# Optimization experiments

Hardware: AMD Instinct MI355X
Metric: run time of the kernel (lower is better)

## Reference

```python
import jax, jax.numpy as jnp
import numpy as np

P = 16      # spatial_size
STEP = 8    # spatial_size // 2 (overlapping)
T = 16      # temporal_size


def setup_inputs() -> dict:
    key = jax.random.key(0)
    k1, k2 = jax.random.split(key)
    inp = jax.random.normal(k1, (8, 4, T, 256, 256), dtype=jnp.float32)
    # reset_parameters: uniform(-1/sqrt(spatial_size), 1/sqrt(spatial_size)) = +/-0.25
    weight = jax.random.uniform(k2, (T, STEP, STEP), dtype=jnp.float32,
                                minval=-0.25, maxval=0.25)
    return {"input": inp, "weight": weight,
            "pad_h": 264, "pad_w": 264, "n_patch_h": 32, "n_patch_w": 32}


def reference(input, weight, pad_h, pad_w, n_patch_h, n_patch_w):
    B, S, Tt, H, W = input.shape
    # zero-pad frames to (pad_h, pad_w) = step*(n_patch+1)
    padded = jnp.pad(input, ((0, 0), (0, 0), (0, 0), (0, pad_h - H), (0, pad_w - W)))
    # tile the (T, step, step) mask over the padded frame
    w_tiled = jnp.tile(weight, (1, n_patch_h + 1, n_patch_w + 1))  # (T, pad_h, pad_w)
    # masked multiply + temporal sum  -> (B, S, pad_h, pad_w)
    out = jnp.einsum('bsthw,thw->bshw', padded, w_tiled)
    # overlapping unfold: windows of size P with stride STEP
    wins_h = (pad_h - P) // STEP + 1
    wins_w = (pad_w - P) // STEP + 1
    rows = (jnp.arange(wins_h) * STEP)[:, None] + jnp.arange(P)  # (wins_h, P)
    cols = (jnp.arange(wins_w) * STEP)[:, None] + jnp.arange(P)  # (wins_w, P)
    # gather patches: (B, S, wins_h, wins_w, P, P)
    patches = out[:, :, rows[:, None, :, None], cols[None, :, None, :]]
    # torch permute(0,1,2,3,5,4): transpose each patch
    patches = jnp.swapaxes(patches, 4, 5)
    # view (B, S*wins_h*wins_w, P*P)
    return patches.reshape(B, -1, P * P)
```

## Files before the change

### kernel.cpp

```cpp
#include <hip/hip_runtime.h>


namespace {

constexpr int TT   = 16;
constexpr int LDSW = 268;

__global__ __launch_bounds__(256, 4) void meas_kernel(
    const float* __restrict__ in, const float* __restrict__ wt,
    float* __restrict__ out)
{
    __shared__ float tile[8 * LDSW];
    __shared__ float wlds[TT * 64];

    const int tid = threadIdx.x;
    for (int idx = tid; idx < TT * 64; idx += 256) wlds[idx] = wt[idx];

    if (tid < 16) {
        const int r  = tid >> 1;
        const int c4 = 64 + (tid & 1);
        *reinterpret_cast<float4*>(&tile[r * LDSW + c4 * 4]) =
            make_float4(0.f, 0.f, 0.f, 0.f);
    }

    const int bid = (blockIdx.x & 7) * 128 + (blockIdx.x >> 3);
    const int g = bid & 31;
    const int s = (bid >> 5) & 3;
    const int b = bid >> 7;

    const float* __restrict__ inp = in + (size_t)(b * 4 + s) * TT * 65536;
    float* __restrict__ outb = out + ((size_t)b * 4096 + (size_t)s * 1024) * 256;

    __syncthreads();

#pragma unroll 1
    for (int m = 0; m < 2; ++m) {
        const int slot = m * 256 + tid;
        const int r = slot >> 6;
        const int c = slot & 63;
        const int h = g * 8 + r;
        const int w = c * 4;
        const float* gp = inp + h * 256 + w;

        float4 v[TT];
#pragma unroll
        for (int t = 0; t < TT; ++t)
            v[t] = *reinterpret_cast<const float4*>(gp + t * 65536);

        __builtin_amdgcn_sched_barrier(0);

        const float* wrow = &wlds[(h & 7) * 8 + (w & 7)];
        float4 acc = make_float4(0.f, 0.f, 0.f, 0.f);
#pragma unroll
        for (int t = 0; t < TT; ++t) {
            const float4 wv = *reinterpret_cast<const float4*>(wrow + t * 64);
            acc.x += v[t].x * wv.x;
            acc.y += v[t].y * wv.y;
            acc.z += v[t].z * wv.z;
            acc.w += v[t].w * wv.w;
        }
        *reinterpret_cast<float4*>(&tile[r * LDSW + w]) = acc;
    }

    __syncthreads();

#pragma unroll
    for (int m2 = 0; m2 < 4; ++m2) {
        const int f  = m2 * 256 + tid;
        const int j  = f >> 5;
        const int e  = f & 31;
        const int q2 = e >> 1;
        const int pp = (e & 1) * 4;
        const float* src = &tile[pp * LDSW + j * 8 + q2];
        const float4 a4 = make_float4(src[0], src[LDSW], src[2 * LDSW], src[3 * LDSW]);

        {
            const int n = 32 * g + j;
            *reinterpret_cast<float4*>(outb + (size_t)n * 256 + q2 * 16 + pp) = a4;
        }
        if (g > 0) {
            const int n = 32 * (g - 1) + j;
            *reinterpret_cast<float4*>(outb + (size_t)n * 256 + q2 * 16 + 8 + pp) = a4;
        }
        if (g == 31) {
            const int n = 992 + j;
            *reinterpret_cast<float4*>(outb + (size_t)n * 256 + q2 * 16 + 8 + pp) =
                make_float4(0.f, 0.f, 0.f, 0.f);
        }
    }
}

}

extern "C" void kernel_launch(void* const* d_in, const int* in_sizes, int n_in,
                              void* d_out, int out_size, void* d_ws, size_t ws_size,
                              hipStream_t stream) {
    const float* in = (const float*)d_in[0];
    const float* wt = (const float*)d_in[1];
    float* out      = (float*)d_out;
    hipLaunchKernelGGL(meas_kernel, dim3(1024), dim3(256), 0, stream, in, wt, out);
}
```

Measured before the change: 31.79 us.

## Split each block's 8-row band into two 4-row half-bands across 2048 blocks

Each block now handles 4 input rows instead of 8, doubling the grid to 2048 blocks and halving the LDS tile. Each thread does one 16-frame load pass instead of two, and occupancy is raised to 5 waves per SIMD. The last half-band block zero-fills the padded bottom patch row up front, and output writes are re-indexed so each half-band fills half of each patch. This aims for more parallelism and latency hiding, at the cost of more block overhead and repeated weight loads into LDS.

```diff
diff --git a/kernel.cpp b/kernel.cpp
--- a/kernel.cpp
+++ b/kernel.cpp
@@ -6,39 +6,48 @@
 constexpr int TT   = 16;
 constexpr int LDSW = 268;
 
-__global__ __launch_bounds__(256, 4) void meas_kernel(
+__global__ __launch_bounds__(256, 5) void meas_kernel(
     const float* __restrict__ in, const float* __restrict__ wt,
     float* __restrict__ out)
 {
-    __shared__ float tile[8 * LDSW];
+    __shared__ float tile[4 * LDSW];
     __shared__ float wlds[TT * 64];
 
     const int tid = threadIdx.x;
     for (int idx = tid; idx < TT * 64; idx += 256) wlds[idx] = wt[idx];
 
-    if (tid < 16) {
+    if (tid < 8) {
         const int r  = tid >> 1;
         const int c4 = 64 + (tid & 1);
         *reinterpret_cast<float4*>(&tile[r * LDSW + c4 * 4]) =
             make_float4(0.f, 0.f, 0.f, 0.f);
     }
 
-    const int bid = (blockIdx.x & 7) * 128 + (blockIdx.x >> 3);
-    const int g = bid & 31;
-    const int s = (bid >> 5) & 3;
-    const int b = bid >> 7;
+    const int bid = (blockIdx.x & 7) * 256 + (blockIdx.x >> 3);
+    const int g = bid & 63;
+    const int s = (bid >> 6) & 3;
+    const int b = bid >> 8;
 
     const float* __restrict__ inp = in + (size_t)(b * 4 + s) * TT * 65536;
     float* __restrict__ outb = out + ((size_t)b * 4096 + (size_t)s * 1024) * 256;
 
+    if (g == 63) {
+        const float4 z4 = make_float4(0.f, 0.f, 0.f, 0.f);
+#pragma unroll
+        for (int m2 = 0; m2 < 4; ++m2) {
+            const int u = m2 * 256 + tid;
+            const int j = u >> 5, e = u & 31;
+            const int q2 = e >> 1, p0 = 8 + (e & 1) * 4;
+            *reinterpret_cast<float4*>(outb + (size_t)(992 + j) * 256 + q2 * 16 + p0) = z4;
+        }
+    }
+
     __syncthreads();
 
-#pragma unroll 1
-    for (int m = 0; m < 2; ++m) {
-        const int slot = m * 256 + tid;
-        const int r = slot >> 6;
-        const int c = slot & 63;
-        const int h = g * 8 + r;
+    {
+        const int r = tid >> 6;
+        const int c = tid & 63;
+        const int h = g * 4 + r;
         const int w = c * 4;
         const float* gp = inp + h * 256 + w;
 
@@ -64,29 +73,19 @@
 
     __syncthreads();
 
+    const int i1  = g >> 1;
+    const int pp0 = (g & 1) * 4;
 #pragma unroll
-    for (int m2 = 0; m2 < 4; ++m2) {
-        const int f  = m2 * 256 + tid;
-        const int j  = f >> 5;
-        const int e  = f & 31;
-        const int q2 = e >> 1;
-        const int pp = (e & 1) * 4;
-        const float* src = &tile[pp * LDSW + j * 8 + q2];
+    for (int m2 = 0; m2 < 2; ++m2) {
+        const int u  = m2 * 256 + tid;
+        const int j  = u >> 4;
+        const int q2 = u & 15;
+        const float* src = &tile[j * 8 + q2];
         const float4 a4 = make_float4(src[0], src[LDSW], src[2 * LDSW], src[3 * LDSW]);
 
-        {
-            const int n = 32 * g + j;
-            *reinterpret_cast<float4*>(outb + (size_t)n * 256 + q2 * 16 + pp) = a4;
-        }
-        if (g > 0) {
-            const int n = 32 * (g - 1) + j;
-            *reinterpret_cast<float4*>(outb + (size_t)n * 256 + q2 * 16 + 8 + pp) = a4;
-        }
-        if (g == 31) {
-            const int n = 992 + j;
-            *reinterpret_cast<float4*>(outb + (size_t)n * 256 + q2 * 16 + 8 + pp) =
-                make_float4(0.f, 0.f, 0.f, 0.f);
-        }
+        *reinterpret_cast<float4*>(outb + (size_t)(i1 * 32 + j) * 256 + q2 * 16 + pp0) = a4;
+        if (i1 > 0)
+            *reinterpret_cast<float4*>(outb + (size_t)((i1 - 1) * 32 + j) * 256 + q2 * 16 + pp0 + 8) = a4;
     }
 }
 
@@ -98,5 +97,5 @@
     const float* in = (const float*)d_in[0];
     const float* wt = (const float*)d_in[1];
     float* out      = (float*)d_out;
-    hipLaunchKernelGGL(meas_kernel, dim3(1024), dim3(256), 0, stream, in, wt, out);
+    hipLaunchKernelGGL(meas_kernel, dim3(2048), dim3(256), 0, stream, in, wt, out);
 }
```

Result: slower. 32.72 us (+2.9%).

## Split tile into two halves and overlap second load with first-half stores

Applied to the files above, without the earlier changes.

The block's 8-row tile is now processed as two 4-row halves held in separate LDS buffers. The second half's global loads are issued before the first half's output stores, so memory reads overlap with writes. The weight load into LDS is also moved after the first input loads are issued, hiding its latency. Plain __syncthreads is replaced by lgkmcnt-only barriers, which avoid waiting on outstanding global loads. The cost is an extra barrier phase and more complex scheduling.

```diff
diff --git a/kernel.cpp b/kernel.cpp
--- a/kernel.cpp
+++ b/kernel.cpp
@@ -6,22 +6,23 @@
 constexpr int TT   = 16;
 constexpr int LDSW = 268;
 
+typedef float fvec4 __attribute__((ext_vector_type(4)));
+
+__device__ __forceinline__ void lgkm_barrier() {
+    __builtin_amdgcn_sched_barrier(0);
+    asm volatile("s_waitcnt lgkmcnt(0)" ::: "memory");
+    __builtin_amdgcn_s_barrier();
+    __builtin_amdgcn_sched_barrier(0);
+}
+
 __global__ __launch_bounds__(256, 4) void meas_kernel(
     const float* __restrict__ in, const float* __restrict__ wt,
     float* __restrict__ out)
 {
-    __shared__ float tile[8 * LDSW];
+    __shared__ float tile[2][4 * LDSW];
     __shared__ float wlds[TT * 64];
 
     const int tid = threadIdx.x;
-    for (int idx = tid; idx < TT * 64; idx += 256) wlds[idx] = wt[idx];
-
-    if (tid < 16) {
-        const int r  = tid >> 1;
-        const int c4 = 64 + (tid & 1);
-        *reinterpret_cast<float4*>(&tile[r * LDSW + c4 * 4]) =
-            make_float4(0.f, 0.f, 0.f, 0.f);
-    }
 
     const int bid = (blockIdx.x & 7) * 128 + (blockIdx.x >> 3);
     const int g = bid & 31;
@@ -31,25 +32,33 @@
     const float* __restrict__ inp = in + (size_t)(b * 4 + s) * TT * 65536;
     float* __restrict__ outb = out + ((size_t)b * 4096 + (size_t)s * 1024) * 256;
 
-    __syncthreads();
+    const int r = tid >> 6;
+    const int c = tid & 63;
+    const int w = c * 4;
+    const int h0 = g * 8 + r;
 
-#pragma unroll 1
-    for (int m = 0; m < 2; ++m) {
-        const int slot = m * 256 + tid;
-        const int r = slot >> 6;
-        const int c = slot & 63;
-        const int h = g * 8 + r;
-        const int w = c * 4;
-        const float* gp = inp + h * 256 + w;
-
-        float4 v[TT];
+    float4 v[TT];
+    {
+        const float* gp = inp + h0 * 256 + w;
 #pragma unroll
         for (int t = 0; t < TT; ++t)
             v[t] = *reinterpret_cast<const float4*>(gp + t * 65536);
+    }
+    __builtin_amdgcn_sched_barrier(0);
 
-        __builtin_amdgcn_sched_barrier(0);
+    for (int idx = tid; idx < TT * 64; idx += 256) wlds[idx] = wt[idx];
+    if (tid < 16) {
+        const int tq = tid >> 3;
+        const int r4 = (tid >> 1) & 3;
+        const int c4 = 64 + (tid & 1);
+        *reinterpret_cast<float4*>(&tile[tq][r4 * LDSW + c4 * 4]) =
+            make_float4(0.f, 0.f, 0.f, 0.f);
+    }
 
-        const float* wrow = &wlds[(h & 7) * 8 + (w & 7)];
+    lgkm_barrier();
+
+    {
+        const float* wrow = &wlds[(h0 & 7) * 8 + (w & 7)];
         float4 acc = make_float4(0.f, 0.f, 0.f, 0.f);
 #pragma unroll
         for (int t = 0; t < TT; ++t) {
@@ -59,34 +68,64 @@
             acc.z += v[t].z * wv.z;
             acc.w += v[t].w * wv.w;
         }
-        *reinterpret_cast<float4*>(&tile[r * LDSW + w]) = acc;
+        *reinterpret_cast<float4*>(&tile[0][r * LDSW + w]) = acc;
     }
 
-    __syncthreads();
+    const int h1 = h0 + 4;
+    {
+        const float* gp = inp + h1 * 256 + w;
+#pragma unroll
+        for (int t = 0; t < TT; ++t)
+            v[t] = *reinterpret_cast<const float4*>(gp + t * 65536);
+    }
+    __builtin_amdgcn_sched_barrier(0);
+
+    lgkm_barrier();
 
 #pragma unroll
-    for (int m2 = 0; m2 < 4; ++m2) {
-        const int f  = m2 * 256 + tid;
-        const int j  = f >> 5;
-        const int e  = f & 31;
-        const int q2 = e >> 1;
-        const int pp = (e & 1) * 4;
-        const float* src = &tile[pp * LDSW + j * 8 + q2];
+    for (int m2 = 0; m2 < 2; ++m2) {
+        const int u  = m2 * 256 + tid;
+        const int j  = u >> 4;
+        const int q2 = u & 15;
+        const float* src = &tile[0][j * 8 + q2];
         const float4 a4 = make_float4(src[0], src[LDSW], src[2 * LDSW], src[3 * LDSW]);
+        *reinterpret_cast<float4*>(outb + (size_t)(g * 32 + j) * 256 + q2 * 16) = a4;
+        if (g > 0)
+            *reinterpret_cast<float4*>(outb + (size_t)((g - 1) * 32 + j) * 256 + q2 * 16 + 8) = a4;
+        if (g == 31)
+            *reinterpret_cast<float4*>(outb + (size_t)(992 + j) * 256 + q2 * 16 + 8) =
+                make_float4(0.f, 0.f, 0.f, 0.f);
+    }
 
-        {
-            const int n = 32 * g + j;
-            *reinterpret_cast<float4*>(outb + (size_t)n * 256 + q2 * 16 + pp) = a4;
+    {
+        const float* wrow = &wlds[(h1 & 7) * 8 + (w & 7)];
+        float4 acc = make_float4(0.f, 0.f, 0.f, 0.f);
+#pragma unroll
+        for (int t = 0; t < TT; ++t) {
+            const float4 wv = *reinterpret_cast<const float4*>(wrow + t * 64);
+            acc.x += v[t].x * wv.x;
+            acc.y += v[t].y * wv.y;
+            acc.z += v[t].z * wv.z;
+            acc.w += v[t].w * wv.w;
         }
-        if (g > 0) {
-            const int n = 32 * (g - 1) + j;
-            *reinterpret_cast<float4*>(outb + (size_t)n * 256 + q2 * 16 + 8 + pp) = a4;
-        }
-        if (g == 31) {
-            const int n = 992 + j;
-            *reinterpret_cast<float4*>(outb + (size_t)n * 256 + q2 * 16 + 8 + pp) =
+        *reinterpret_cast<float4*>(&tile[1][r * LDSW + w]) = acc;
+    }
+
+    lgkm_barrier();
+
+#pragma unroll
+    for (int m2 = 0; m2 < 2; ++m2) {
+        const int u  = m2 * 256 + tid;
+        const int j  = u >> 4;
+        const int q2 = u & 15;
+        const float* src = &tile[1][j * 8 + q2];
+        const float4 a4 = make_float4(src[0], src[LDSW], src[2 * LDSW], src[3 * LDSW]);
+        *reinterpret_cast<float4*>(outb + (size_t)(g * 32 + j) * 256 + q2 * 16 + 4) = a4;
+        if (g > 0)
+            *reinterpret_cast<float4*>(outb + (size_t)((g - 1) * 32 + j) * 256 + q2 * 16 + 12) = a4;
+        if (g == 31)
+            *reinterpret_cast<float4*>(outb + (size_t)(992 + j) * 256 + q2 * 16 + 12) =
                 make_float4(0.f, 0.f, 0.f, 0.f);
-        }
     }
 }
 
```

Result: slower. 34.22 us (+7.7%).
